# Performance work log

Measured on AMD Instinct MI355X. Metric: run time of the kernel, lower is better.

## Reference

```python
import jax, jax.numpy as jnp
import numpy as np

C = 32            # multiplicity per irrep (node irreps = 32x0e + 32x1o)
N_NODES = 50000
N_EDGES = 800000
R_DIM = 8         # radial embedding dim
R_HID = 8         # radial MLP hidden width
N_SPECIES = 5
AVG_NEIGH = 16.0
N_PATHS = 4       # 0ex0e->0e, 0ex1o->1o, 1ox0e->1o, 1ox1o->0e


def setup_inputs() -> dict:
    key = jax.random.key(0)
    ks = jax.random.split(key, 16)
    inp = {
        'node_features': jax.random.normal(ks[0], (N_NODES, 4 * C), jnp.float32),
        'edge_features': jax.random.normal(ks[1], (N_EDGES, 4), jnp.float32),
        'radial_embedding': jax.random.normal(ks[2], (N_EDGES, R_DIM), jnp.float32),
        'senders': jax.random.randint(ks[3], (N_EDGES,), 0, N_NODES),
        'receivers': jax.random.randint(ks[4], (N_EDGES,), 0, N_NODES),
        'node_species': jax.random.randint(ks[5], (N_NODES,), 0, N_SPECIES),
        # linear_up: per-irrep (block-diagonal) mixing
        'W_up_s': jax.random.normal(ks[6], (C, C), jnp.float32),
        'W_up_v': jax.random.normal(ks[7], (C, C), jnp.float32),
        # radial MLP (no biases, e3nn-style): R_DIM -> R_HID -> N_PATHS*C
        'W_r1': jax.random.normal(ks[8], (R_DIM, R_HID), jnp.float32),
        'W_r2': jax.random.normal(ks[9], (R_HID, N_PATHS * C), jnp.float32),
        # linear_down: 2C x 0e -> 2C (C feats + C gates); 2C x 1o -> C x 1o
        'W_down_s': jax.random.normal(ks[10], (2 * C, 2 * C), jnp.float32),
        'W_down_v': jax.random.normal(ks[11], (2 * C, C), jnp.float32),
        # species-indexed skip connection to gate irreps
        'W_skip_s': jax.random.normal(ks[12], (N_SPECIES, C, 2 * C), jnp.float32),
        'W_skip_v': jax.random.normal(ks[13], (N_SPECIES, C, C), jnp.float32),
    }
    return inp


def reference(node_features, edge_features, radial_embedding, senders, receivers,
              node_species, W_up_s, W_up_v, W_r1, W_r2, W_down_s, W_down_v,
              W_skip_s, W_skip_v):
    N = node_features.shape[0]
    inv_sqrt_C = 1.0 / np.sqrt(C)
    # split irreps: scalars [N,C] and vectors [N,C,3]
    s = node_features[:, :C]
    v = node_features[:, C:].reshape(N, C, 3)
    # ---- linear_up (block-diagonal irreps Linear, fan-in normalized) ----
    s_up = (s @ W_up_s) * inv_sqrt_C
    v_up = jnp.einsum('ncx,cd->ndx', v, W_up_v) * inv_sqrt_C
    # ---- radial MLP -> per-edge tensor-product path weights ----
    h = jax.nn.silu((radial_embedding @ W_r1) * (1.0 / np.sqrt(R_DIM)))
    w = ((h @ W_r2) * (1.0 / np.sqrt(R_HID))).reshape(-1, N_PATHS, C)  # [E,4,C]
    # ---- tensor product messages over edges ----
    sh0 = edge_features[:, 0]      # [E]  l=0
    sh1 = edge_features[:, 1:4]    # [E,3] l=1
    se = s_up[senders]             # [E,C]
    ve = v_up[senders]             # [E,C,3]
    m0 = jnp.concatenate([
        w[:, 0] * se * sh0[:, None],                                      # 0e x 0e -> 0e
        w[:, 3] * jnp.einsum('ecx,ex->ec', ve, sh1) * (1.0 / np.sqrt(3.0))  # 1o x 1o -> 0e
    ], axis=1)                                                            # [E,2C]
    m1 = jnp.concatenate([
        w[:, 1, :, None] * se[:, :, None] * sh1[:, None, :],              # 0e x 1o -> 1o
        w[:, 2, :, None] * ve * sh0[:, None, None],                       # 1o x 0e -> 1o
    ], axis=1)                                                            # [E,2C,3]
    # ---- scatter aggregate to receivers, normalize by sqrt(avg neigh) ----
    inv_sqrt_deg = 1.0 / np.sqrt(AVG_NEIGH)
    agg0 = jax.ops.segment_sum(m0, receivers, num_segments=N) * inv_sqrt_deg
    agg1 = jax.ops.segment_sum(m1, receivers, num_segments=N) * inv_sqrt_deg
    # ---- linear_down to gate irreps (2C x 0e: C feats + C gates; C x 1o) ----
    inv_sqrt_2C = 1.0 / np.sqrt(2 * C)
    sc = (agg0 @ W_down_s) * inv_sqrt_2C                     # [N,2C]
    vc = jnp.einsum('ncx,cd->ndx', agg1, W_down_v) * inv_sqrt_2C  # [N,C,3]
    # ---- species-indexed skip connection ----
    skip_s = jnp.einsum('nc,ncd->nd', s, W_skip_s[node_species]) * inv_sqrt_C
    skip_v = jnp.einsum('ncx,ncd->ndx', v, W_skip_v[node_species]) * inv_sqrt_C
    sc = 0.5 * (sc + skip_s)
    vc = 0.5 * (vc + skip_v)
    # ---- gated nonlinearity: silu on scalars, silu(gates) * vectors ----
    feats = jax.nn.silu(sc[:, :C])
    gates = jax.nn.silu(sc[:, C:])
    vg = vc * gates[:, :, None]
    return jnp.concatenate([feats, vg.reshape(N, 3 * C)], axis=1)  # [N,4C]
```

## Files before the change

### kernel.cpp

```cpp
#include <hip/hip_runtime.h>
#include <stdint.h>

__device__ __forceinline__ float b2f(unsigned short u) {
    union { uint32_t i; float f; } v; v.i = ((uint32_t)u) << 16; return v.f;
}
__device__ __forceinline__ unsigned short f2b(float f) {
    union { float f; uint32_t i; } v; v.f = f;
    uint32_t i = v.i;
    uint32_t r = (i + 0x7fffu + ((i >> 16) & 1u)) >> 16;
    return (unsigned short)r;
}
__device__ __forceinline__ float silu_f(float x) { return x / (1.f + __expf(-x)); }

template<bool BF>
__device__ __forceinline__ float ldin(const void* p, size_t i) {
    if (BF) return b2f(((const unsigned short*)p)[i]);
    return ((const float*)p)[i];
}
template<bool BF>
__device__ __forceinline__ void ld4(const void* p, size_t i, float o[4]) {
    if (BF) {
        const ushort4 u = *(const ushort4*)((const unsigned short*)p + i);
        o[0] = b2f(u.x); o[1] = b2f(u.y); o[2] = b2f(u.z); o[3] = b2f(u.w);
    } else {
        const float4 f = *(const float4*)((const float*)p + i);
        o[0] = f.x; o[1] = f.y; o[2] = f.z; o[3] = f.w;
    }
}
template<bool BF>
__device__ __forceinline__ void stout(void* p, size_t i, float v) {
    if (BF) ((unsigned short*)p)[i] = f2b(v);
    else    ((float*)p)[i] = v;
}

#define INV_SQRT_C   0.17677669529663687f
#define INV_SQRT_8   0.3535533905932738f
#define INV_SQRT_3   0.5773502691896258f
#define INV_SQRT_DEG 0.25f
#define INV_SQRT_2C  0.125f

__device__ __forceinline__ bool detect_bf(const void* nf) {
    const int lane = threadIdx.x & 63;
    const uint32_t w = ((const uint32_t*)nf)[lane];
    const uint32_t ex = (w >> 7) & 0xFFu;
    const unsigned long long m = __ballot(ex >= 96u && ex <= 130u);
    return __popcll(m) > 32;
}

template<bool BF>
__device__ __forceinline__ void prep_body(
    const void* __restrict__ nf, const void* __restrict__ Wus,
    const void* __restrict__ Wuv, const void* __restrict__ radial,
    const int* __restrict__ recv, const void* __restrict__ Wr1,
    unsigned short* __restrict__ stage, unsigned short* __restrict__ hbuf,
    int* __restrict__ counts, int* __restrict__ table,
    int* __restrict__ ovcnt, int* __restrict__ ovlist, int N, int E)
{
    const int tid = threadIdx.x;
    __shared__ float sin_[256];
    const int half = tid >> 7;
    const int t = tid & 127;
    const int npairs = (N + 1) >> 1;
    for (int pair = blockIdx.x; pair < npairs; pair += gridDim.x) {
        const int n = pair * 2 + half;
        __syncthreads();
        if (n < N) sin_[half * 128 + t] = ldin<BF>(nf, (size_t)n * 128 + t);
        __syncthreads();
        if (n < N) {
            const float* sb = &sin_[half * 128];
            float acc = 0.f;
            if (t < 32) {
                #pragma unroll 8
                for (int c = 0; c < 32; ++c) acc += sb[c] * ldin<BF>(Wus, c * 32 + t);
                stage[(size_t)n * 128 + t] = f2b(acc * INV_SQRT_C);
            } else {
                const int q = t - 32;
                const int x = q >> 5;
                const int d = q & 31;
                #pragma unroll 8
                for (int c = 0; c < 32; ++c) acc += sb[32 + c * 3 + x] * ldin<BF>(Wuv, c * 32 + d);
                stage[(size_t)n * 128 + 32 + x * 32 + d] = f2b(acc * INV_SQRT_C);
            }
        }
    }
    for (int base = blockIdx.x * 256; base < E; base += gridDim.x * 256) {
        const int e = base + tid;
        if (e >= E) continue;
        float r[8];
        ld4<BF>(radial, (size_t)e * 8, r);
        ld4<BF>(radial, (size_t)e * 8 + 4, r + 4);
        unsigned short h[8];
        #pragma unroll
        for (int j = 0; j < 8; ++j) {
            float pre = 0.f;
            #pragma unroll
            for (int k = 0; k < 8; ++k) pre += r[k] * ldin<BF>(Wr1, k * 8 + j);
            pre *= INV_SQRT_8;
            h[j] = f2b(silu_f(pre) * INV_SQRT_8);
        }
        ushort4* hp = (ushort4*)(hbuf + (size_t)e * 8);
        hp[0] = make_ushort4(h[0], h[1], h[2], h[3]);
        hp[1] = make_ushort4(h[4], h[5], h[6], h[7]);
        const int rr = recv[e];
        const int pos = atomicAdd(&counts[rr], 1);
        if (pos < 64) table[(size_t)rr * 64 + pos] = e;
        else          ovlist[atomicAdd(ovcnt, 1)] = e;
    }
}
__global__ __launch_bounds__(256) void k_prep(
    const void* nf, const void* Wus, const void* Wuv, const void* radial,
    const int* recv, const void* Wr1,
    unsigned short* stage, unsigned short* hbuf,
    int* counts, int* table, int* ovcnt, int* ovlist, int N, int E)
{
    if (detect_bf(nf)) prep_body<true >(nf, Wus, Wuv, radial, recv, Wr1, stage, hbuf,
                                        counts, table, ovcnt, ovlist, N, E);
    else               prep_body<false>(nf, Wus, Wuv, radial, recv, Wr1, stage, hbuf,
                                        counts, table, ovcnt, ovlist, N, E);
}

template<bool BF>
__device__ __forceinline__ void aggregate_body(
    const void* __restrict__ nf, const void* __restrict__ ef,
    const int* __restrict__ senders, const int* __restrict__ recv,
    const int* __restrict__ species,
    const void* __restrict__ Wr2, const void* __restrict__ Wds,
    const void* __restrict__ Wdv, const void* __restrict__ Wss,
    const void* __restrict__ Wsv,
    const unsigned short* __restrict__ stage,
    const unsigned short* __restrict__ hbuf,
    const int* __restrict__ counts, const int* __restrict__ table,
    const int* __restrict__ ovcnt, const int* __restrict__ ovlist,
    void* __restrict__ out, int N)
{
    __shared__ float lds_agg0[4][64];
    __shared__ float lds_agg1[4][3][65];
    __shared__ float lds_scf[4][64];
    const int wave = threadIdx.x >> 6;
    const int lane = threadIdx.x & 63;
    const int n = blockIdx.x * 4 + wave;
    const bool valid = (n < N);
    int sp = 0;

    if (valid) {
        sp = species[n];
        const int cnt = counts[n];

        const int colA = (lane < 32) ? lane : lane + 32;
        float wA[8], wB[8];
        #pragma unroll
        for (int j = 0; j < 8; ++j) {
            wA[j] = ldin<BF>(Wr2, j * 128 + colA);
            wB[j] = ldin<BF>(Wr2, j * 128 + colA + 32);
        }

        const int mc = (cnt < 64) ? cnt : 64;
        int snd_r = 0;
        uint32_t ef0 = 0, ef1 = 0, ef2 = 0, ef3 = 0;
        uint32_t h0 = 0, h1 = 0, h2 = 0, h3 = 0;
        if (lane < mc) {
            const int eid = table[(size_t)n * 64 + lane];
            snd_r = senders[eid];
            if (BF) {
                const uint2 t = *(const uint2*)((const unsigned short*)ef + (size_t)eid * 4);
                ef0 = t.x; ef1 = t.y;
            } else {
                const uint4 t = *(const uint4*)((const float*)ef + (size_t)eid * 4);
                ef0 = t.x; ef1 = t.y; ef2 = t.z; ef3 = t.w;
            }
            const uint4 th = *(const uint4*)(hbuf + (size_t)eid * 8);
            h0 = th.x; h1 = th.y; h2 = th.z; h3 = th.w;
        }

        float acc0 = 0.f, a1x = 0.f, a1y = 0.f, a1z = 0.f;
        const int d = lane - 32;

        unsigned short c0 = 0, c1 = 0, c2 = 0;
        if (mc > 0) {
            const int s0 = __shfl(snd_r, 0, 64);
            const unsigned short* rec = stage + (size_t)s0 * 128;
            if (lane < 32) { c0 = rec[lane]; }
            else { c0 = rec[32 + d]; c1 = rec[64 + d]; c2 = rec[96 + d]; }
        }
        #pragma unroll 2
        for (int i = 0; i < mc; ++i) {
            unsigned short n0 = 0, n1 = 0, n2 = 0;
            if (i + 1 < mc) {
                const int sn = __shfl(snd_r, i + 1, 64);
                const unsigned short* rec = stage + (size_t)sn * 128;
                if (lane < 32) { n0 = rec[lane]; }
                else { n0 = rec[32 + d]; n1 = rec[64 + d]; n2 = rec[96 + d]; }
            }
            float sh0, s1x, s1y, s1z;
            if (BF) {
                const uint32_t a = (uint32_t)__shfl((int)ef0, i, 64);
                const uint32_t b = (uint32_t)__shfl((int)ef1, i, 64);
                sh0 = b2f((unsigned short)(a & 0xFFFFu)); s1x = b2f((unsigned short)(a >> 16));
                s1y = b2f((unsigned short)(b & 0xFFFFu)); s1z = b2f((unsigned short)(b >> 16));
            } else {
                sh0 = __int_as_float(__shfl((int)ef0, i, 64));
                s1x = __int_as_float(__shfl((int)ef1, i, 64));
                s1y = __int_as_float(__shfl((int)ef2, i, 64));
                s1z = __int_as_float(__shfl((int)ef3, i, 64));
            }
            const uint32_t ua = (uint32_t)__shfl((int)h0, i, 64);
            const uint32_t ub = (uint32_t)__shfl((int)h1, i, 64);
            const uint32_t uc = (uint32_t)__shfl((int)h2, i, 64);
            const uint32_t ud = (uint32_t)__shfl((int)h3, i, 64);
            float h[8];
            h[0] = b2f((unsigned short)(ua & 0xFFFFu)); h[1] = b2f((unsigned short)(ua >> 16));
            h[2] = b2f((unsigned short)(ub & 0xFFFFu)); h[3] = b2f((unsigned short)(ub >> 16));
            h[4] = b2f((unsigned short)(uc & 0xFFFFu)); h[5] = b2f((unsigned short)(uc >> 16));
            h[6] = b2f((unsigned short)(ud & 0xFFFFu)); h[7] = b2f((unsigned short)(ud >> 16));
            const float vA = h[0] * wA[0] + h[1] * wA[1] + h[2] * wA[2] + h[3] * wA[3]
                           + h[4] * wA[4] + h[5] * wA[5] + h[6] * wA[6] + h[7] * wA[7];
            const float vB = h[0] * wB[0] + h[1] * wB[1] + h[2] * wB[2] + h[3] * wB[3]
                           + h[4] * wB[4] + h[5] * wB[5] + h[6] * wB[6] + h[7] * wB[7];
            if (lane < 32) {
                const float se = b2f(c0);
                acc0 += vA * se * sh0;
                const float tt = vB * se;
                a1x += tt * s1x; a1y += tt * s1y; a1z += tt * s1z;
            } else {
                const float vx = b2f(c0), vy = b2f(c1), vz = b2f(c2);
                acc0 += vB * (vx * s1x + vy * s1y + vz * s1z) * INV_SQRT_3;
                const float tt = vA * sh0;
                a1x += tt * vx; a1y += tt * vy; a1z += tt * vz;
            }
            c0 = n0; c1 = n1; c2 = n2;
        }
        if (cnt > 64) {
            const int oc = *ovcnt;
            for (int i2 = 0; i2 < oc; ++i2) {
                const int e = ovlist[i2];
                if (recv[e] != n) continue;
                const int s = senders[e];
                float efv[4];
                ld4<BF>(ef, (size_t)e * 4, efv);
                const float sh0 = efv[0], s1x = efv[1], s1y = efv[2], s1z = efv[3];
                float h[8];
                #pragma unroll
                for (int j = 0; j < 8; ++j) h[j] = b2f(hbuf[(size_t)e * 8 + j]);
                const float vA = h[0] * wA[0] + h[1] * wA[1] + h[2] * wA[2] + h[3] * wA[3]
                               + h[4] * wA[4] + h[5] * wA[5] + h[6] * wA[6] + h[7] * wA[7];
                const float vB = h[0] * wB[0] + h[1] * wB[1] + h[2] * wB[2] + h[3] * wB[3]
                               + h[4] * wB[4] + h[5] * wB[5] + h[6] * wB[6] + h[7] * wB[7];
                const unsigned short* rec = stage + (size_t)s * 128;
                if (lane < 32) {
                    const float se = b2f(rec[lane]);
                    acc0 += vA * se * sh0;
                    const float tt = vB * se;
                    a1x += tt * s1x; a1y += tt * s1y; a1z += tt * s1z;
                } else {
                    const float vx = b2f(rec[32 + d]), vy = b2f(rec[64 + d]), vz = b2f(rec[96 + d]);
                    acc0 += vB * (vx * s1x + vy * s1y + vz * s1z) * INV_SQRT_3;
                    const float tt = vA * sh0;
                    a1x += tt * vx; a1y += tt * vy; a1z += tt * vz;
                }
            }
        }
        lds_agg0[wave][lane]    = acc0 * INV_SQRT_DEG;
        lds_agg1[wave][0][lane] = a1x * INV_SQRT_DEG;
        lds_agg1[wave][1][lane] = a1y * INV_SQRT_DEG;
        lds_agg1[wave][2][lane] = a1z * INV_SQRT_DEG;
    }
    __syncthreads();
    if (valid) {
        float sc = 0.f;
        #pragma unroll 8
        for (int c = 0; c < 64; ++c) sc += lds_agg0[wave][c] * ldin<BF>(Wds, c * 64 + lane);
        sc *= INV_SQRT_2C;
        float ss = 0.f;
        #pragma unroll 8
        for (int c = 0; c < 32; ++c)
            ss += ldin<BF>(nf, (size_t)n * 128 + c) * ldin<BF>(Wss, (size_t)sp * 2048 + c * 64 + lane);
        ss *= INV_SQRT_C;
        lds_scf[wave][lane] = 0.5f * (sc + ss);
    }
    __syncthreads();
    if (valid) {
        #pragma unroll
        for (int rr = 0; rr < 2; ++rr) {
            const int p = lane + rr * 64;
            float outv;
            if (p < 32) {
                outv = silu_f(lds_scf[wave][p]);
            } else {
                const int o = p - 32;
                const int c = o / 3;
                const int x = o - 3 * c;
                float vc = 0.f;
                #pragma unroll 8
                for (int c2 = 0; c2 < 64; ++c2) vc += lds_agg1[wave][x][c2] * ldin<BF>(Wdv, c2 * 32 + c);
                vc *= INV_SQRT_2C;
                float sv = 0.f;
                #pragma unroll 8
                for (int c2 = 0; c2 < 32; ++c2)
                    sv += ldin<BF>(nf, (size_t)n * 128 + 32 + c2 * 3 + x) * ldin<BF>(Wsv, (size_t)sp * 1024 + c2 * 32 + c);
                sv *= INV_SQRT_C;
                const float g = silu_f(lds_scf[wave][32 + c]);
                outv = 0.5f * (vc + sv) * g;
            }
            stout<BF>(out, (size_t)n * 128 + p, outv);
        }
    }
}
__global__ __launch_bounds__(256) void k_aggregate(
    const void* nf, const void* ef, const int* senders, const int* recv,
    const int* species,
    const void* Wr2, const void* Wds, const void* Wdv, const void* Wss, const void* Wsv,
    const unsigned short* stage, const unsigned short* hbuf,
    const int* counts, const int* table, const int* ovcnt, const int* ovlist,
    void* out, int N)
{
    if (detect_bf(nf)) aggregate_body<true >(nf, ef, senders, recv, species,
                                             Wr2, Wds, Wdv, Wss, Wsv,
                                             stage, hbuf, counts, table, ovcnt, ovlist, out, N);
    else               aggregate_body<false>(nf, ef, senders, recv, species,
                                             Wr2, Wds, Wdv, Wss, Wsv,
                                             stage, hbuf, counts, table, ovcnt, ovlist, out, N);
}

extern "C" void kernel_launch(void* const* d_in, const int* in_sizes, int n_in,
                              void* d_out, int out_size, void* d_ws, size_t ws_size,
                              hipStream_t stream) {
    const void* nf      = d_in[0];
    const void* ef      = d_in[1];
    const void* radial  = d_in[2];
    const int*  senders = (const int*)d_in[3];
    const int*  recv    = (const int*)d_in[4];
    const int*  specie  = (const int*)d_in[5];
    const void* Wus = d_in[6];
    const void* Wuv = d_in[7];
    const void* Wr1 = d_in[8];
    const void* Wr2 = d_in[9];
    const void* Wds = d_in[10];
    const void* Wdv = d_in[11];
    const void* Wss = d_in[12];
    const void* Wsv = d_in[13];

    const int N = in_sizes[5];
    const int E = in_sizes[3];

    const size_t stageB = (size_t)N * 128 * 2;
    const size_t hbufB  = (size_t)E * 8 * 2;
    const size_t tableB = (size_t)N * 64 * 4;
    const size_t need   = stageB + hbufB + tableB + (size_t)(N + 1 + E) * 4;
    if (ws_size < need) return;

    char* ws = (char*)d_ws;
    unsigned short* stage = (unsigned short*)ws;
    unsigned short* hbuf  = (unsigned short*)(ws + stageB);
    int* table   = (int*)(ws + stageB + hbufB);
    int* counts  = (int*)(ws + stageB + hbufB + tableB);
    int* ovcnt   = counts + N;
    int* ovlist  = ovcnt + 1;

    hipMemsetAsync(counts, 0, (size_t)(N + 1) * sizeof(int), stream);

    k_prep<<<2048, 256, 0, stream>>>(nf, Wus, Wuv, radial, recv, Wr1,
                                     stage, hbuf, counts, table, ovcnt, ovlist, N, E);
    k_aggregate<<<(N + 3) / 4, 256, 0, stream>>>(nf, ef, senders, recv, specie,
                                                 Wr2, Wds, Wdv, Wss, Wsv,
                                                 stage, hbuf, counts, table, ovcnt, ovlist,
                                                 d_out, N);
}
```

Before: 449.8 us.

## Fuse memset, prep and aggregate into one cooperative persistent kernel

```diff
diff --git a/kernel.cpp b/kernel.cpp
--- a/kernel.cpp
+++ b/kernel.cpp
@@ -1,5 +1,8 @@
 #include <hip/hip_runtime.h>
+#include <hip/hip_cooperative_groups.h>
 #include <stdint.h>
+
+namespace cg = cooperative_groups;
 
 __device__ __forceinline__ float b2f(unsigned short u) {
     union { uint32_t i; float f; } v; v.i = ((uint32_t)u) << 16; return v.f;
@@ -48,7 +51,7 @@
 }
 
 template<bool BF>
-__device__ __forceinline__ void prep_body(
+__device__ __forceinline__ void prep_phase(
     const void* __restrict__ nf, const void* __restrict__ Wus,
     const void* __restrict__ Wuv, const void* __restrict__ radial,
     const int* __restrict__ recv, const void* __restrict__ Wr1,
@@ -107,20 +110,10 @@
         else          ovlist[atomicAdd(ovcnt, 1)] = e;
     }
 }
-__global__ __launch_bounds__(256) void k_prep(
-    const void* nf, const void* Wus, const void* Wuv, const void* radial,
-    const int* recv, const void* Wr1,
-    unsigned short* stage, unsigned short* hbuf,
-    int* counts, int* table, int* ovcnt, int* ovlist, int N, int E)
-{
-    if (detect_bf(nf)) prep_body<true >(nf, Wus, Wuv, radial, recv, Wr1, stage, hbuf,
-                                        counts, table, ovcnt, ovlist, N, E);
-    else               prep_body<false>(nf, Wus, Wuv, radial, recv, Wr1, stage, hbuf,
-                                        counts, table, ovcnt, ovlist, N, E);
-}
-
-template<bool BF>
-__device__ __forceinline__ void aggregate_body(
+
+template<bool BF>
+__device__ __forceinline__ void agg_group(
+    int g,
     const void* __restrict__ nf, const void* __restrict__ ef,
     const int* __restrict__ senders, const int* __restrict__ recv,
     const int* __restrict__ species,
@@ -138,14 +131,13 @@
     __shared__ float lds_scf[4][64];
     const int wave = threadIdx.x >> 6;
     const int lane = threadIdx.x & 63;
-    const int n = blockIdx.x * 4 + wave;
+    const int n = g * 4 + wave;
     const bool valid = (n < N);
     int sp = 0;
 
     if (valid) {
         sp = species[n];
         const int cnt = counts[n];
-
         const int colA = (lane < 32) ? lane : lane + 32;
         float wA[8], wB[8];
         #pragma unroll
@@ -298,27 +290,75 @@
                 for (int c2 = 0; c2 < 32; ++c2)
                     sv += ldin<BF>(nf, (size_t)n * 128 + 32 + c2 * 3 + x) * ldin<BF>(Wsv, (size_t)sp * 1024 + c2 * 32 + c);
                 sv *= INV_SQRT_C;
-                const float g = silu_f(lds_scf[wave][32 + c]);
-                outv = 0.5f * (vc + sv) * g;
+                const float g2 = silu_f(lds_scf[wave][32 + c]);
+                outv = 0.5f * (vc + sv) * g2;
             }
             stout<BF>(out, (size_t)n * 128 + p, outv);
         }
     }
+    __syncthreads();
+}
+
+template<bool BF>
+__device__ __forceinline__ void fused_body(
+    const void* nf, const void* ef, const void* radial,
+    const int* senders, const int* recv, const int* species,
+    const void* Wus, const void* Wuv, const void* Wr1, const void* Wr2,
+    const void* Wds, const void* Wdv, const void* Wss, const void* Wsv,
+    unsigned short* stage, unsigned short* hbuf,
+    int* counts, int* table, int* ovlist, void* out, int N, int E)
+{
+    cg::grid_group grid = cg::this_grid();
+    int* ovcnt = counts + N;
+    for (int i = blockIdx.x * 256 + threadIdx.x; i <= N; i += gridDim.x * 256) counts[i] = 0;
+    __threadfence();
+    grid.sync();
+    prep_phase<BF>(nf, Wus, Wuv, radial, recv, Wr1, stage, hbuf, counts, table, ovcnt, ovlist, N, E);
+    __threadfence();
+    grid.sync();
+    const int ngroups = (N + 3) >> 2;
+    for (int g = blockIdx.x; g < ngroups; g += gridDim.x)
+        agg_group<BF>(g, nf, ef, senders, recv, species, Wr2, Wds, Wdv, Wss, Wsv,
+                      stage, hbuf, counts, table, ovcnt, ovlist, out, N);
+}
+__global__ __launch_bounds__(256) void k_fused(
+    const void* nf, const void* ef, const void* radial,
+    const int* senders, const int* recv, const int* species,
+    const void* Wus, const void* Wuv, const void* Wr1, const void* Wr2,
+    const void* Wds, const void* Wdv, const void* Wss, const void* Wsv,
+    unsigned short* stage, unsigned short* hbuf,
+    int* counts, int* table, int* ovlist, void* out, int N, int E)
+{
+    if (detect_bf(nf)) fused_body<true >(nf, ef, radial, senders, recv, species,
+                                         Wus, Wuv, Wr1, Wr2, Wds, Wdv, Wss, Wsv,
+                                         stage, hbuf, counts, table, ovlist, out, N, E);
+    else               fused_body<false>(nf, ef, radial, senders, recv, species,
+                                         Wus, Wuv, Wr1, Wr2, Wds, Wdv, Wss, Wsv,
+                                         stage, hbuf, counts, table, ovlist, out, N, E);
+}
+
+__global__ __launch_bounds__(256) void k_prep(
+    const void* nf, const void* Wus, const void* Wuv, const void* radial,
+    const int* recv, const void* Wr1,
+    unsigned short* stage, unsigned short* hbuf,
+    int* counts, int* table, int* ovlist, int N, int E)
+{
+    int* ovcnt = counts + N;
+    if (detect_bf(nf)) prep_phase<true >(nf, Wus, Wuv, radial, recv, Wr1, stage, hbuf, counts, table, ovcnt, ovlist, N, E);
+    else               prep_phase<false>(nf, Wus, Wuv, radial, recv, Wr1, stage, hbuf, counts, table, ovcnt, ovlist, N, E);
 }
 __global__ __launch_bounds__(256) void k_aggregate(
     const void* nf, const void* ef, const int* senders, const int* recv,
     const int* species,
     const void* Wr2, const void* Wds, const void* Wdv, const void* Wss, const void* Wsv,
     const unsigned short* stage, const unsigned short* hbuf,
-    const int* counts, const int* table, const int* ovcnt, const int* ovlist,
-    void* out, int N)
-{
-    if (detect_bf(nf)) aggregate_body<true >(nf, ef, senders, recv, species,
-                                             Wr2, Wds, Wdv, Wss, Wsv,
-                                             stage, hbuf, counts, table, ovcnt, ovlist, out, N);
-    else               aggregate_body<false>(nf, ef, senders, recv, species,
-                                             Wr2, Wds, Wdv, Wss, Wsv,
-                                             stage, hbuf, counts, table, ovcnt, ovlist, out, N);
+    const int* counts, const int* table, const int* ovlist, void* out, int N)
+{
+    const int* ovcnt = counts + N;
+    if (detect_bf(nf)) agg_group<true >(blockIdx.x, nf, ef, senders, recv, species,
+                                        Wr2, Wds, Wdv, Wss, Wsv, stage, hbuf, counts, table, ovcnt, ovlist, out, N);
+    else               agg_group<false>(blockIdx.x, nf, ef, senders, recv, species,
+                                        Wr2, Wds, Wdv, Wss, Wsv, stage, hbuf, counts, table, ovcnt, ovlist, out, N);
 }
 
 extern "C" void kernel_launch(void* const* d_in, const int* in_sizes, int n_in,
@@ -339,8 +379,8 @@
     const void* Wss = d_in[12];
     const void* Wsv = d_in[13];
 
-    const int N = in_sizes[5];
-    const int E = in_sizes[3];
+    int N = in_sizes[5];
+    int E = in_sizes[3];
 
     const size_t stageB = (size_t)N * 128 * 2;
     const size_t hbufB  = (size_t)E * 8 * 2;
@@ -353,15 +393,25 @@
     unsigned short* hbuf  = (unsigned short*)(ws + stageB);
     int* table   = (int*)(ws + stageB + hbufB);
     int* counts  = (int*)(ws + stageB + hbufB + tableB);
-    int* ovcnt   = counts + N;
-    int* ovlist  = ovcnt + 1;
-
-    hipMemsetAsync(counts, 0, (size_t)(N + 1) * sizeof(int), stream);
-
-    k_prep<<<2048, 256, 0, stream>>>(nf, Wus, Wuv, radial, recv, Wr1,
-                                     stage, hbuf, counts, table, ovcnt, ovlist, N, E);
-    k_aggregate<<<(N + 3) / 4, 256, 0, stream>>>(nf, ef, senders, recv, specie,
-                                                 Wr2, Wds, Wdv, Wss, Wsv,
-                                                 stage, hbuf, counts, table, ovcnt, ovlist,
-                                                 d_out, N);
-}
+    int* ovlist  = counts + N + 1;
+
+    void* args[] = { (void*)&nf, (void*)&ef, (void*)&radial,
+                     (void*)&senders, (void*)&recv, (void*)&specie,
+                     (void*)&Wus, (void*)&Wuv, (void*)&Wr1, (void*)&Wr2,
+                     (void*)&Wds, (void*)&Wdv, (void*)&Wss, (void*)&Wsv,
+                     (void*)&stage, (void*)&hbuf,
+                     (void*)&counts, (void*)&table, (void*)&ovlist,
+                     (void*)&d_out, (void*)&N, (void*)&E };
+    hipError_t err = hipLaunchCooperativeKernel((const void*)k_fused,
+                                                dim3(1024), dim3(256),
+                                                args, 0, stream);
+    if (err != hipSuccess) {
+        hipMemsetAsync(counts, 0, (size_t)(N + 1) * sizeof(int), stream);
+        k_prep<<<2048, 256, 0, stream>>>(nf, Wus, Wuv, radial, recv, Wr1,
+                                         stage, hbuf, counts, table, ovlist, N, E);
+        k_aggregate<<<(N + 3) / 4, 256, 0, stream>>>(nf, ef, senders, recv, specie,
+                                                     Wr2, Wds, Wdv, Wss, Wsv,
+                                                     stage, hbuf, counts, table, ovlist,
+                                                     d_out, N);
+    }
+}
```

After: 1.016 ms. 126% more time.

## Pack per-edge sender, features and radial hidden into one record; deepen prefetch

Applied to the files above, without the earlier changes.

```diff
diff --git a/kernel.cpp b/kernel.cpp
--- a/kernel.cpp
+++ b/kernel.cpp
@@ -48,11 +48,12 @@
 }
 
 template<bool BF>
-__device__ __forceinline__ void prep_body(
+__device__ __forceinline__ void prep_phase(
     const void* __restrict__ nf, const void* __restrict__ Wus,
     const void* __restrict__ Wuv, const void* __restrict__ radial,
+    const void* __restrict__ ef, const int* __restrict__ senders,
     const int* __restrict__ recv, const void* __restrict__ Wr1,
-    unsigned short* __restrict__ stage, unsigned short* __restrict__ hbuf,
+    unsigned short* __restrict__ stage, uint4* __restrict__ epack,
     int* __restrict__ counts, int* __restrict__ table,
     int* __restrict__ ovcnt, int* __restrict__ ovlist, int N, int E)
 {
@@ -98,9 +99,25 @@
             pre *= INV_SQRT_8;
             h[j] = f2b(silu_f(pre) * INV_SQRT_8);
         }
-        ushort4* hp = (ushort4*)(hbuf + (size_t)e * 8);
-        hp[0] = make_ushort4(h[0], h[1], h[2], h[3]);
-        hp[1] = make_ushort4(h[4], h[5], h[6], h[7]);
+        uint32_t ef01, ef23;
+        if (BF) {
+            const uint2 tv = *(const uint2*)((const unsigned short*)ef + (size_t)e * 4);
+            ef01 = tv.x; ef23 = tv.y;
+        } else {
+            const float4 fv = *(const float4*)((const float*)ef + (size_t)e * 4);
+            ef01 = (uint32_t)f2b(fv.x) | ((uint32_t)f2b(fv.y) << 16);
+            ef23 = (uint32_t)f2b(fv.z) | ((uint32_t)f2b(fv.w) << 16);
+        }
+        const uint32_t snd = (uint32_t)senders[e];
+        uint4 a, b;
+        a.x = snd; a.y = ef01; a.z = ef23;
+        a.w = (uint32_t)h[0] | ((uint32_t)h[1] << 16);
+        b.x = (uint32_t)h[2] | ((uint32_t)h[3] << 16);
+        b.y = (uint32_t)h[4] | ((uint32_t)h[5] << 16);
+        b.z = (uint32_t)h[6] | ((uint32_t)h[7] << 16);
+        b.w = 0;
+        epack[(size_t)e * 2]     = a;
+        epack[(size_t)e * 2 + 1] = b;
         const int rr = recv[e];
         const int pos = atomicAdd(&counts[rr], 1);
         if (pos < 64) table[(size_t)rr * 64 + pos] = e;
@@ -109,26 +126,68 @@
 }
 __global__ __launch_bounds__(256) void k_prep(
     const void* nf, const void* Wus, const void* Wuv, const void* radial,
-    const int* recv, const void* Wr1,
-    unsigned short* stage, unsigned short* hbuf,
-    int* counts, int* table, int* ovcnt, int* ovlist, int N, int E)
+    const void* ef, const int* senders, const int* recv, const void* Wr1,
+    unsigned short* stage, uint4* epack,
+    int* counts, int* table, int* ovlist, int N, int E)
 {
-    if (detect_bf(nf)) prep_body<true >(nf, Wus, Wuv, radial, recv, Wr1, stage, hbuf,
-                                        counts, table, ovcnt, ovlist, N, E);
-    else               prep_body<false>(nf, Wus, Wuv, radial, recv, Wr1, stage, hbuf,
-                                        counts, table, ovcnt, ovlist, N, E);
-}
-
-template<bool BF>
-__device__ __forceinline__ void aggregate_body(
-    const void* __restrict__ nf, const void* __restrict__ ef,
-    const int* __restrict__ senders, const int* __restrict__ recv,
+    int* ovcnt = counts + N;
+    if (detect_bf(nf)) prep_phase<true >(nf, Wus, Wuv, radial, ef, senders, recv, Wr1,
+                                         stage, epack, counts, table, ovcnt, ovlist, N, E);
+    else               prep_phase<false>(nf, Wus, Wuv, radial, ef, senders, recv, Wr1,
+                                         stage, epack, counts, table, ovcnt, ovlist, N, E);
+}
+
+#define STAGE_LOAD(k, B0, B1, B2) do { \
+    const int sk_ = __shfl(snd_r, (k), 64); \
+    const unsigned short* rec_ = stage + (size_t)sk_ * 128; \
+    if (lane < 32) { B0 = rec_[lane]; } \
+    else { B0 = rec_[32 + d]; B1 = rec_[64 + d]; B2 = rec_[96 + d]; } \
+} while (0)
+
+#define EDGE_BODY(i, B0, B1, B2) do { \
+    const uint32_t a_ = (uint32_t)__shfl((int)ef0, (i), 64); \
+    const uint32_t bb_ = (uint32_t)__shfl((int)ef1, (i), 64); \
+    const float sh0 = b2f((unsigned short)(a_ & 0xFFFFu)); \
+    const float s1x = b2f((unsigned short)(a_ >> 16)); \
+    const float s1y = b2f((unsigned short)(bb_ & 0xFFFFu)); \
+    const float s1z = b2f((unsigned short)(bb_ >> 16)); \
+    const uint32_t ua = (uint32_t)__shfl((int)h0, (i), 64); \
+    const uint32_t ub = (uint32_t)__shfl((int)h1, (i), 64); \
+    const uint32_t uc = (uint32_t)__shfl((int)h2, (i), 64); \
+    const uint32_t ud = (uint32_t)__shfl((int)h3, (i), 64); \
+    float hh[8]; \
+    hh[0] = b2f((unsigned short)(ua & 0xFFFFu)); hh[1] = b2f((unsigned short)(ua >> 16)); \
+    hh[2] = b2f((unsigned short)(ub & 0xFFFFu)); hh[3] = b2f((unsigned short)(ub >> 16)); \
+    hh[4] = b2f((unsigned short)(uc & 0xFFFFu)); hh[5] = b2f((unsigned short)(uc >> 16)); \
+    hh[6] = b2f((unsigned short)(ud & 0xFFFFu)); hh[7] = b2f((unsigned short)(ud >> 16)); \
+    const float vA = hh[0]*wA[0]+hh[1]*wA[1]+hh[2]*wA[2]+hh[3]*wA[3] \
+                   + hh[4]*wA[4]+hh[5]*wA[5]+hh[6]*wA[6]+hh[7]*wA[7]; \
+    const float vB = hh[0]*wB[0]+hh[1]*wB[1]+hh[2]*wB[2]+hh[3]*wB[3] \
+                   + hh[4]*wB[4]+hh[5]*wB[5]+hh[6]*wB[6]+hh[7]*wB[7]; \
+    if (lane < 32) { \
+        const float se = b2f((unsigned short)(B0)); \
+        acc0 += vA * se * sh0; \
+        const float tt = vB * se; \
+        a1x += tt * s1x; a1y += tt * s1y; a1z += tt * s1z; \
+    } else { \
+        const float vx = b2f((unsigned short)(B0)); \
+        const float vy = b2f((unsigned short)(B1)); \
+        const float vz = b2f((unsigned short)(B2)); \
+        acc0 += vB * (vx * s1x + vy * s1y + vz * s1z) * INV_SQRT_3; \
+        const float tt = vA * sh0; \
+        a1x += tt * vx; a1y += tt * vy; a1z += tt * vz; \
+    } \
+} while (0)
+
+template<bool BF>
+__device__ __forceinline__ void agg_body(
+    const void* __restrict__ nf, const int* __restrict__ recv,
     const int* __restrict__ species,
     const void* __restrict__ Wr2, const void* __restrict__ Wds,
     const void* __restrict__ Wdv, const void* __restrict__ Wss,
     const void* __restrict__ Wsv,
     const unsigned short* __restrict__ stage,
-    const unsigned short* __restrict__ hbuf,
+    const uint4* __restrict__ epack,
     const int* __restrict__ counts, const int* __restrict__ table,
     const int* __restrict__ ovcnt, const int* __restrict__ ovlist,
     void* __restrict__ out, int N)
@@ -145,7 +204,6 @@
     if (valid) {
         sp = species[n];
         const int cnt = counts[n];
-
         const int colA = (lane < 32) ? lane : lane + 32;
         float wA[8], wB[8];
         #pragma unroll
@@ -156,96 +214,57 @@
 
         const int mc = (cnt < 64) ? cnt : 64;
         int snd_r = 0;
-        uint32_t ef0 = 0, ef1 = 0, ef2 = 0, ef3 = 0;
-        uint32_t h0 = 0, h1 = 0, h2 = 0, h3 = 0;
+        uint32_t ef0 = 0, ef1 = 0, h0 = 0, h1 = 0, h2 = 0, h3 = 0;
         if (lane < mc) {
             const int eid = table[(size_t)n * 64 + lane];
-            snd_r = senders[eid];
-            if (BF) {
-                const uint2 t = *(const uint2*)((const unsigned short*)ef + (size_t)eid * 4);
-                ef0 = t.x; ef1 = t.y;
-            } else {
-                const uint4 t = *(const uint4*)((const float*)ef + (size_t)eid * 4);
-                ef0 = t.x; ef1 = t.y; ef2 = t.z; ef3 = t.w;
-            }
-            const uint4 th = *(const uint4*)(hbuf + (size_t)eid * 8);
-            h0 = th.x; h1 = th.y; h2 = th.z; h3 = th.w;
+            const uint4 a = epack[(size_t)eid * 2];
+            const uint4 b = epack[(size_t)eid * 2 + 1];
+            snd_r = (int)a.x; ef0 = a.y; ef1 = a.z;
+            h0 = a.w; h1 = b.x; h2 = b.y; h3 = b.z;
         }
 
         float acc0 = 0.f, a1x = 0.f, a1y = 0.f, a1z = 0.f;
         const int d = lane - 32;
-
-        unsigned short c0 = 0, c1 = 0, c2 = 0;
-        if (mc > 0) {
-            const int s0 = __shfl(snd_r, 0, 64);
-            const unsigned short* rec = stage + (size_t)s0 * 128;
-            if (lane < 32) { c0 = rec[lane]; }
-            else { c0 = rec[32 + d]; c1 = rec[64 + d]; c2 = rec[96 + d]; }
-        }
-        #pragma unroll 2
-        for (int i = 0; i < mc; ++i) {
-            unsigned short n0 = 0, n1 = 0, n2 = 0;
-            if (i + 1 < mc) {
-                const int sn = __shfl(snd_r, i + 1, 64);
-                const unsigned short* rec = stage + (size_t)sn * 128;
-                if (lane < 32) { n0 = rec[lane]; }
-                else { n0 = rec[32 + d]; n1 = rec[64 + d]; n2 = rec[96 + d]; }
+        const int mcp = (mc + 3) & ~3;
+
+        uint32_t c0a=0,c1a=0,c2a=0, c0b=0,c1b=0,c2b=0,
+                 c0c=0,c1c=0,c2c=0, c0d=0,c1d=0,c2d=0;
+        if (mcp > 0) {
+            STAGE_LOAD(0, c0a, c1a, c2a);
+            if (1 < mcp) STAGE_LOAD(1, c0b, c1b, c2b);
+            if (2 < mcp) STAGE_LOAD(2, c0c, c1c, c2c);
+            for (int i = 0; i + 4 <= mcp; i += 4) {
+                STAGE_LOAD(i + 3, c0d, c1d, c2d);
+                EDGE_BODY(i, c0a, c1a, c2a);
+                if (i + 4 < mcp) STAGE_LOAD(i + 4, c0a, c1a, c2a);
+                EDGE_BODY(i + 1, c0b, c1b, c2b);
+                if (i + 5 < mcp) STAGE_LOAD(i + 5, c0b, c1b, c2b);
+                EDGE_BODY(i + 2, c0c, c1c, c2c);
+                if (i + 6 < mcp) STAGE_LOAD(i + 6, c0c, c1c, c2c);
+                EDGE_BODY(i + 3, c0d, c1d, c2d);
             }
-            float sh0, s1x, s1y, s1z;
-            if (BF) {
-                const uint32_t a = (uint32_t)__shfl((int)ef0, i, 64);
-                const uint32_t b = (uint32_t)__shfl((int)ef1, i, 64);
-                sh0 = b2f((unsigned short)(a & 0xFFFFu)); s1x = b2f((unsigned short)(a >> 16));
-                s1y = b2f((unsigned short)(b & 0xFFFFu)); s1z = b2f((unsigned short)(b >> 16));
-            } else {
-                sh0 = __int_as_float(__shfl((int)ef0, i, 64));
-                s1x = __int_as_float(__shfl((int)ef1, i, 64));
-                s1y = __int_as_float(__shfl((int)ef2, i, 64));
-                s1z = __int_as_float(__shfl((int)ef3, i, 64));
-            }
-            const uint32_t ua = (uint32_t)__shfl((int)h0, i, 64);
-            const uint32_t ub = (uint32_t)__shfl((int)h1, i, 64);
-            const uint32_t uc = (uint32_t)__shfl((int)h2, i, 64);
-            const uint32_t ud = (uint32_t)__shfl((int)h3, i, 64);
-            float h[8];
-            h[0] = b2f((unsigned short)(ua & 0xFFFFu)); h[1] = b2f((unsigned short)(ua >> 16));
-            h[2] = b2f((unsigned short)(ub & 0xFFFFu)); h[3] = b2f((unsigned short)(ub >> 16));
-            h[4] = b2f((unsigned short)(uc & 0xFFFFu)); h[5] = b2f((unsigned short)(uc >> 16));
-            h[6] = b2f((unsigned short)(ud & 0xFFFFu)); h[7] = b2f((unsigned short)(ud >> 16));
-            const float vA = h[0] * wA[0] + h[1] * wA[1] + h[2] * wA[2] + h[3] * wA[3]
-                           + h[4] * wA[4] + h[5] * wA[5] + h[6] * wA[6] + h[7] * wA[7];
-            const float vB = h[0] * wB[0] + h[1] * wB[1] + h[2] * wB[2] + h[3] * wB[3]
-                           + h[4] * wB[4] + h[5] * wB[5] + h[6] * wB[6] + h[7] * wB[7];
-            if (lane < 32) {
-                const float se = b2f(c0);
-                acc0 += vA * se * sh0;
-                const float tt = vB * se;
-                a1x += tt * s1x; a1y += tt * s1y; a1z += tt * s1z;
-            } else {
-                const float vx = b2f(c0), vy = b2f(c1), vz = b2f(c2);
-                acc0 += vB * (vx * s1x + vy * s1y + vz * s1z) * INV_SQRT_3;
-                const float tt = vA * sh0;
-                a1x += tt * vx; a1y += tt * vy; a1z += tt * vz;
-            }
-            c0 = n0; c1 = n1; c2 = n2;
         }
         if (cnt > 64) {
             const int oc = *ovcnt;
             for (int i2 = 0; i2 < oc; ++i2) {
                 const int e = ovlist[i2];
                 if (recv[e] != n) continue;
-                const int s = senders[e];
-                float efv[4];
-                ld4<BF>(ef, (size_t)e * 4, efv);
-                const float sh0 = efv[0], s1x = efv[1], s1y = efv[2], s1z = efv[3];
-                float h[8];
-                #pragma unroll
-                for (int j = 0; j < 8; ++j) h[j] = b2f(hbuf[(size_t)e * 8 + j]);
-                const float vA = h[0] * wA[0] + h[1] * wA[1] + h[2] * wA[2] + h[3] * wA[3]
-                               + h[4] * wA[4] + h[5] * wA[5] + h[6] * wA[6] + h[7] * wA[7];
-                const float vB = h[0] * wB[0] + h[1] * wB[1] + h[2] * wB[2] + h[3] * wB[3]
-                               + h[4] * wB[4] + h[5] * wB[5] + h[6] * wB[6] + h[7] * wB[7];
-                const unsigned short* rec = stage + (size_t)s * 128;
+                const uint4 a = epack[(size_t)e * 2];
+                const uint4 b = epack[(size_t)e * 2 + 1];
+                const float sh0 = b2f((unsigned short)(a.y & 0xFFFFu));
+                const float s1x = b2f((unsigned short)(a.y >> 16));
+                const float s1y = b2f((unsigned short)(a.z & 0xFFFFu));
+                const float s1z = b2f((unsigned short)(a.z >> 16));
+                float hh[8];
+                hh[0] = b2f((unsigned short)(a.w & 0xFFFFu)); hh[1] = b2f((unsigned short)(a.w >> 16));
+                hh[2] = b2f((unsigned short)(b.x & 0xFFFFu)); hh[3] = b2f((unsigned short)(b.x >> 16));
+                hh[4] = b2f((unsigned short)(b.y & 0xFFFFu)); hh[5] = b2f((unsigned short)(b.y >> 16));
+                hh[6] = b2f((unsigned short)(b.z & 0xFFFFu)); hh[7] = b2f((unsigned short)(b.z >> 16));
+                const float vA = hh[0]*wA[0]+hh[1]*wA[1]+hh[2]*wA[2]+hh[3]*wA[3]
+                               + hh[4]*wA[4]+hh[5]*wA[5]+hh[6]*wA[6]+hh[7]*wA[7];
+                const float vB = hh[0]*wB[0]+hh[1]*wB[1]+hh[2]*wB[2]+hh[3]*wB[3]
+                               + hh[4]*wB[4]+hh[5]*wB[5]+hh[6]*wB[6]+hh[7]*wB[7];
+                const unsigned short* rec = stage + (size_t)a.x * 128;
                 if (lane < 32) {
                     const float se = b2f(rec[lane]);
                     acc0 += vA * se * sh0;
@@ -298,27 +317,24 @@
                 for (int c2 = 0; c2 < 32; ++c2)
                     sv += ldin<BF>(nf, (size_t)n * 128 + 32 + c2 * 3 + x) * ldin<BF>(Wsv, (size_t)sp * 1024 + c2 * 32 + c);
                 sv *= INV_SQRT_C;
-                const float g = silu_f(lds_scf[wave][32 + c]);
-                outv = 0.5f * (vc + sv) * g;
+                const float g2 = silu_f(lds_scf[wave][32 + c]);
+                outv = 0.5f * (vc + sv) * g2;
             }
             stout<BF>(out, (size_t)n * 128 + p, outv);
         }
     }
 }
 __global__ __launch_bounds__(256) void k_aggregate(
-    const void* nf, const void* ef, const int* senders, const int* recv,
-    const int* species,
+    const void* nf, const int* recv, const int* species,
     const void* Wr2, const void* Wds, const void* Wdv, const void* Wss, const void* Wsv,
-    const unsigned short* stage, const unsigned short* hbuf,
-    const int* counts, const int* table, const int* ovcnt, const int* ovlist,
-    void* out, int N)
+    const unsigned short* stage, const uint4* epack,
+    const int* counts, const int* table, const int* ovlist, void* out, int N)
 {
-    if (detect_bf(nf)) aggregate_body<true >(nf, ef, senders, recv, species,
-                                             Wr2, Wds, Wdv, Wss, Wsv,
-                                             stage, hbuf, counts, table, ovcnt, ovlist, out, N);
-    else               aggregate_body<false>(nf, ef, senders, recv, species,
-                                             Wr2, Wds, Wdv, Wss, Wsv,
-                                             stage, hbuf, counts, table, ovcnt, ovlist, out, N);
+    const int* ovcnt = counts + N;
+    if (detect_bf(nf)) agg_body<true >(nf, recv, species, Wr2, Wds, Wdv, Wss, Wsv,
+                                       stage, epack, counts, table, ovcnt, ovlist, out, N);
+    else               agg_body<false>(nf, recv, species, Wr2, Wds, Wdv, Wss, Wsv,
+                                       stage, epack, counts, table, ovcnt, ovlist, out, N);
 }
 
 extern "C" void kernel_launch(void* const* d_in, const int* in_sizes, int n_in,
@@ -343,25 +359,23 @@
     const int E = in_sizes[3];
 
     const size_t stageB = (size_t)N * 128 * 2;
-    const size_t hbufB  = (size_t)E * 8 * 2;
+    const size_t epackB = (size_t)E * 32;
     const size_t tableB = (size_t)N * 64 * 4;
-    const size_t need   = stageB + hbufB + tableB + (size_t)(N + 1 + E) * 4;
+    const size_t need   = stageB + epackB + tableB + (size_t)(N + 1 + E) * 4;
     if (ws_size < need) return;
 
     char* ws = (char*)d_ws;
     unsigned short* stage = (unsigned short*)ws;
-    unsigned short* hbuf  = (unsigned short*)(ws + stageB);
-    int* table   = (int*)(ws + stageB + hbufB);
-    int* counts  = (int*)(ws + stageB + hbufB + tableB);
-    int* ovcnt   = counts + N;
-    int* ovlist  = ovcnt + 1;
+    uint4* epack = (uint4*)(ws + stageB);
+    int* table   = (int*)(ws + stageB + epackB);
+    int* counts  = (int*)(ws + stageB + epackB + tableB);
+    int* ovlist  = counts + N + 1;
 
     hipMemsetAsync(counts, 0, (size_t)(N + 1) * sizeof(int), stream);
-
-    k_prep<<<2048, 256, 0, stream>>>(nf, Wus, Wuv, radial, recv, Wr1,
-                                     stage, hbuf, counts, table, ovcnt, ovlist, N, E);
-    k_aggregate<<<(N + 3) / 4, 256, 0, stream>>>(nf, ef, senders, recv, specie,
+    k_prep<<<2048, 256, 0, stream>>>(nf, Wus, Wuv, radial, ef, senders, recv, Wr1,
+                                     stage, epack, counts, table, ovlist, N, E);
+    k_aggregate<<<(N + 3) / 4, 256, 0, stream>>>(nf, recv, specie,
                                                  Wr2, Wds, Wdv, Wss, Wsv,
-                                                 stage, hbuf, counts, table, ovcnt, ovlist,
+                                                 stage, epack, counts, table, ovlist,
                                                  d_out, N);
 }
```

Result: no change. 450.4 us (+0.1%).
